# Performance work log

Measured on AMD Instinct MI355X. Metric: run time of the kernel, lower is better.

## Reference

```python
import jax, jax.numpy as jnp
import numpy as np

B, T, HOR, N = 64, 12, 12, 1024
DIN, DOUT, YCOV, H, K, E = 1, 1, 1, 64, 3, 8


def setup_inputs() -> dict:
    key = jax.random.key(0)
    ks = jax.random.split(key, 10)
    def g(k, shape, s=1.0):
        return jax.random.normal(k, shape, dtype=jnp.float32) * s
    # xavier-ish scale for GCN weights: 1/sqrt(fan_in)
    gi = 1.0 / np.sqrt(K * (DIN + H))
    di = 1.0 / np.sqrt(K * (DOUT + YCOV + H))
    return {
        "x": jax.random.uniform(ks[0], (B, T, N, DIN), dtype=jnp.float32),
        "y_cov": jax.random.uniform(ks[1], (B, HOR, N, YCOV), dtype=jnp.float32),
        "node_emb": g(ks[2], (N, E), 1.0),
        "enc_gate_W": g(ks[3], (K * (DIN + H), 2 * H), gi),
        "enc_gate_b": jnp.zeros((2 * H,), jnp.float32),
        "enc_upd_W": g(ks[4], (K * (DIN + H), H), gi),
        "enc_upd_b": jnp.zeros((H,), jnp.float32),
        "dec_gate_W": g(ks[5], (K * (DOUT + YCOV + H), 2 * H), di),
        "dec_gate_b": jnp.zeros((2 * H,), jnp.float32),
        "dec_upd_W": g(ks[6], (K * (DOUT + YCOV + H), H), di),
        "dec_upd_b": jnp.zeros((H,), jnp.float32),
        "proj_W": g(ks[7], (H, DOUT), 1.0 / np.sqrt(H)),
        "proj_b": jnp.zeros((DOUT,), jnp.float32),
    }


def _cheb_supports(A):
    # support_set = [I, A, 2*A@A - I, ...], cheb_k terms
    s = [jnp.eye(A.shape[0], dtype=A.dtype), A]
    for _ in range(2, K):
        s.append(2.0 * A @ s[-1] - s[-2])
    return jnp.stack(s)  # [K, N, N]


def _gcn(x, sup, W, b):
    # x: [B,N,C]; sup: [K,N,N]; matches torch cat([s_k @ x], -1) ordering (k-major)
    bb, nn, cc = x.shape
    xg = jnp.einsum('knm,bmc->bnkc', sup, x).reshape(bb, nn, K * cc)
    return xg @ W + b


def _cell(x, h, sup, gW, gb, uW, ub):
    zr = jax.nn.sigmoid(_gcn(jnp.concatenate([x, h], -1), sup, gW, gb))
    z, r = jnp.split(zr, 2, axis=-1)
    hc = jnp.tanh(_gcn(jnp.concatenate([x, z * h], -1), sup, uW, ub))
    return r * h + (1.0 - r) * hc


def reference(x, y_cov, node_emb, enc_gate_W, enc_gate_b, enc_upd_W, enc_upd_b,
              dec_gate_W, dec_gate_b, dec_upd_W, dec_upd_b, proj_W, proj_b):
    # adaptive adjacency from node embeddings (AGCRN-style)
    A = jax.nn.softmax(jax.nn.relu(node_emb @ node_emb.T), axis=-1)
    sup = _cheb_supports(A)

    h0 = jnp.zeros((B, N, H), x.dtype)

    def enc_step(h, xt):
        h2 = _cell(xt, h, sup, enc_gate_W, enc_gate_b, enc_upd_W, enc_upd_b)
        return h2, None
    h_enc, _ = jax.lax.scan(enc_step, h0, jnp.swapaxes(x, 0, 1))  # final state [B,N,H]

    go0 = jnp.zeros((B, N, DOUT), x.dtype)

    def dec_step(carry, yt):
        h, go = carry
        h2 = _cell(jnp.concatenate([go, yt], -1), h, sup,
                   dec_gate_W, dec_gate_b, dec_upd_W, dec_upd_b)
        go2 = h2 @ proj_W + proj_b
        return (h2, go2), go2
    _, outs = jax.lax.scan(dec_step, (h_enc, go0), jnp.swapaxes(y_cov, 0, 1))
    return jnp.swapaxes(outs, 0, 1)  # [B, HOR, N, DOUT]
```

## Files before the change

### kernel.cpp

```cpp
#include <hip/hip_runtime.h>
#include <math.h>

constexpr int N = 1024, B = 64, T = 12, HOR = 12, H = 64, E = 8;
constexpr size_t NBH = 4194304;

constexpr size_t A_off   = 0;
constexpr size_t Pxy_off = 1048576;
constexpr size_t h_off   = Pxy_off + 3145728;
constexpr size_t Ph_off  = h_off + NBH;
constexpr size_t zh_off  = Ph_off + 2 * NBH;
constexpr size_t r_off   = zh_off + NBH;
constexpr size_t go_off  = r_off + NBH;
constexpr size_t A2_off  = go_off + 65536;
constexpr size_t Bth_off = A2_off + 1048576;
constexpr size_t Btz_off = Bth_off + 2162688;
constexpr size_t xyK_off = Btz_off + 2097152;
constexpr size_t Pgo_off = xyK_off + 786432;
constexpr size_t wp_off  = Pgo_off + 131072;

typedef __attribute__((ext_vector_type(8))) short short8;
typedef _Float16 half8 __attribute__((ext_vector_type(8)));
typedef __attribute__((ext_vector_type(4))) float f32x4;

__device__ __forceinline__ unsigned f2bf(float x) {
  unsigned u = __float_as_uint(x);
  return (u + 0x7fffu + ((u >> 16) & 1u)) >> 16;
}
__device__ __forceinline__ float bf2f(unsigned h) {
  return __uint_as_float(h << 16);
}
__device__ __forceinline__ ushort f2h(float x) {
  _Float16 h = (_Float16)x;
  ushort u;
  __builtin_memcpy(&u, &h, 2);
  return u;
}
__device__ __forceinline__ void split4(float4 v, uint2& hi, uint2& lo) {
  unsigned h0 = f2bf(v.x), h1 = f2bf(v.y), h2 = f2bf(v.z), h3 = f2bf(v.w);
  unsigned l0 = f2bf(v.x - bf2f(h0)), l1 = f2bf(v.y - bf2f(h1));
  unsigned l2 = f2bf(v.z - bf2f(h2)), l3 = f2bf(v.w - bf2f(h3));
  hi.x = (h0 & 0xffffu) | (h1 << 16); hi.y = (h2 & 0xffffu) | (h3 << 16);
  lo.x = (l0 & 0xffffu) | (l1 << 16); lo.y = (l2 & 0xffffu) | (l3 << 16);
}

typedef const __attribute__((address_space(1))) void gas_t;
typedef __attribute__((address_space(3))) void las_t;

__global__ __launch_bounds__(256) void build_A(const float* __restrict__ emb,
                                               float* __restrict__ A) {
  __shared__ float sE[N * E];
  __shared__ float sv[N];
  __shared__ float rmax[4], rsum[4];
  const int i = blockIdx.x;
  for (int idx = threadIdx.x; idx < N * E / 4; idx += 256)
    ((float4*)sE)[idx] = ((const float4*)emb)[idx];
  __syncthreads();
  float ei[E];
#pragma unroll
  for (int e = 0; e < E; ++e) ei[e] = sE[i * E + e];
  float mymax = 0.f;
  for (int j = threadIdx.x; j < N; j += 256) {
    float d = 0.f;
#pragma unroll
    for (int e = 0; e < E; ++e) d = fmaf(ei[e], sE[j * E + e], d);
    d = fmaxf(d, 0.f);
    sv[j] = d;
    mymax = fmaxf(mymax, d);
  }
  for (int off = 32; off; off >>= 1) mymax = fmaxf(mymax, __shfl_down(mymax, off));
  const int wid = threadIdx.x >> 6, lid = threadIdx.x & 63;
  if (lid == 0) rmax[wid] = mymax;
  __syncthreads();
  const float m = fmaxf(fmaxf(rmax[0], rmax[1]), fmaxf(rmax[2], rmax[3]));
  float mysum = 0.f;
  for (int j = threadIdx.x; j < N; j += 256) {
    float ev = expf(sv[j] - m);
    sv[j] = ev;
    mysum += ev;
  }
  for (int off = 32; off; off >>= 1) mysum += __shfl_down(mysum, off);
  if (lid == 0) rsum[wid] = mysum;
  __syncthreads();
  const float inv = 1.f / (rsum[0] + rsum[1] + rsum[2] + rsum[3]);
  for (int j = threadIdx.x; j < N; j += 256) A[i * N + j] = sv[j] * inv;
}

__global__ __launch_bounds__(256) void pack_split_S(const float* __restrict__ A,
                                                    ushort* __restrict__ L,
                                                    ushort* __restrict__ R) {
  __shared__ float tile[32][33];
  const int bx = blockIdx.x * 32;
  const int by = blockIdx.y * 32;
  const int tx = threadIdx.x & 31;
  const int tg = threadIdx.x >> 5;
#pragma unroll
  for (int p = 0; p < 4; ++p) {
    int ty = tg * 4 + p;
    tile[ty][tx] = A[(size_t)(by + ty) * 1024 + bx + tx];
  }
  __syncthreads();
#pragma unroll
  for (int p = 0; p < 4; ++p) {
    int ty = tg * 4 + p;
    float v = tile[ty][tx];
    unsigned h = f2bf(v);
    unsigned l = f2bf(v - bf2f(h));
    size_t lb = (size_t)(by + ty) * 3072 + 3 * (bx + tx);
    L[lb + 0] = (ushort)h; L[lb + 1] = (ushort)l; L[lb + 2] = (ushort)h;
    float w = tile[tx][ty];
    unsigned hh = f2bf(w);
    unsigned ll = f2bf(w - bf2f(hh));
    size_t rbi = (size_t)(bx + ty) * 3072 + 3 * (by + tx);
    R[rbi + 0] = (ushort)hh; R[rbi + 1] = (ushort)hh; R[rbi + 2] = (ushort)ll;
  }
}

__global__ __launch_bounds__(256) void conv_bf16(const float* __restrict__ src,
                                                 ushort* __restrict__ dst) {
  int i = blockIdx.x * 256 + threadIdx.x;
  float4 v = ((const float4*)src)[i];
  ushort4 o;
  o.x = (ushort)f2bf(v.x); o.y = (ushort)f2bf(v.y);
  o.z = (ushort)f2bf(v.z); o.w = (ushort)f2bf(v.w);
  ((ushort4*)dst)[i] = o;
}

__global__ __launch_bounds__(256) void conv_xyK(const float* __restrict__ src,
                                                ushort* __restrict__ dst, int off) {
  int id = blockIdx.x * 256 + threadIdx.x;
  int tb = id >> 10, n = id & 1023;
  int tt = tb >> 6, b = tb & 63;
  dst[(size_t)(off + tb) * 1024 + n] = (ushort)f2bf(src[((size_t)b * T + tt) * 1024 + n]);
}

__global__ __launch_bounds__(256) void pack_Wbf(const float* __restrict__ W,
                                                ushort* __restrict__ out,
                                                int CIN, int NC, int xoff) {
  int idx = blockIdx.x * 256 + threadIdx.x;
  int total = 2 * NC * 32;
  if (idx >= total) return;
  int kk = idx & 31;
  int rest = idx >> 5;
  int col = rest % NC;
  int half = rest / NC;
  float v = W[(size_t)(xoff + half * 32 + kk) * NC + col];
  unsigned hi = f2bf(v);
  unsigned lo = f2bf(v - bf2f(hi));
  size_t base = (size_t)(half * 2) * NC * 32;
  out[base + (size_t)col * 32 + kk] = (ushort)hi;
  out[base + (size_t)NC * 32 + (size_t)col * 32 + kk] = (ushort)lo;
}

__global__ __launch_bounds__(256) void pack_W16(const float* __restrict__ W,
                                                ushort* __restrict__ out,
                                                int CIN, int NC, int xoff) {
  int idx = blockIdx.x * 256 + threadIdx.x;
  int total = 2 * 2 * NC * 32;
  if (idx >= total) return;
  int kk = idx & 31;
  int rest = idx >> 5;
  int col = rest % NC;
  rest /= NC;
  int half = rest & 1;
  int s1 = rest >> 1;
  int s = s1 + 1;
  float v = W[(size_t)(s * CIN + xoff + half * 32 + kk) * NC + col];
  out[(size_t)(s1 * 2 + half) * NC * 32 + (size_t)col * 32 + kk] = f2h(v);
}

__global__ __launch_bounds__(256) void gemm_s2p(
    const ushort* __restrict__ L, const ushort* __restrict__ R,
    float* __restrict__ P) {
  __shared__ ushort As[128 * 32];
  __shared__ ushort Bs[128 * 32];
  const int t = threadIdx.x;
  const int wave = t >> 6, lane = t & 63;
  const int bm = blockIdx.y * 128, bn = blockIdx.x * 128;
  const int wm = (wave & 1) * 64, wn = (wave >> 1) * 64;
  float* Pz = P + (size_t)blockIdx.z * 1048576;
  const int kbase = blockIdx.z * 768;

  const ushort* aSrc[2]; const ushort* bSrc[2];
  ushort* aDst[2]; ushort* bDst[2];
#pragma unroll
  for (int u = 0; u < 2; ++u) {
    int idx = wave * 128 + u * 64 + lane;
    int row = idx >> 2;
    int kq = (idx & 3) * 8;
    aSrc[u] = L + (size_t)(bm + row) * 3072 + kq;
    bSrc[u] = R + (size_t)(bn + row) * 3072 + kq;
    aDst[u] = &As[(wave * 128 + u * 64) * 8];
    bDst[u] = &Bs[(wave * 128 + u * 64) * 8];
  }
  const int lr = lane & 15;
  const int lk = (lane >> 4) * 8;
  f32x4 acc[4][4];
#pragma unroll
  for (int i = 0; i < 4; ++i)
#pragma unroll
    for (int j = 0; j < 4; ++j) acc[i][j] = {0.f, 0.f, 0.f, 0.f};

  for (int k0 = kbase; k0 < kbase + 768; k0 += 32) {
#pragma unroll
    for (int u = 0; u < 2; ++u) {
      __builtin_amdgcn_global_load_lds((gas_t*)(aSrc[u] + k0), (las_t*)aDst[u], 16, 0, 0);
      __builtin_amdgcn_global_load_lds((gas_t*)(bSrc[u] + k0), (las_t*)bDst[u], 16, 0, 0);
    }
    __syncthreads();
    short8 a[4], b[4];
#pragma unroll
    for (int i = 0; i < 4; ++i) a[i] = *(const short8*)&As[(wm + i * 16 + lr) * 32 + lk];
#pragma unroll
    for (int j = 0; j < 4; ++j) b[j] = *(const short8*)&Bs[(wn + j * 16 + lr) * 32 + lk];
#pragma unroll
    for (int i = 0; i < 4; ++i)
#pragma unroll
      for (int j = 0; j < 4; ++j)
        acc[i][j] = __builtin_amdgcn_mfma_f32_16x16x32_bf16(a[i], b[j], acc[i][j], 0, 0, 0);
    __syncthreads();
  }
  const int cr = (lane >> 4) * 4;
  const int cc = lane & 15;
#pragma unroll
  for (int i = 0; i < 4; ++i)
#pragma unroll
    for (int j = 0; j < 4; ++j) {
      int gm = bm + wm + i * 16 + cr;
      int gn = bn + wn + j * 16 + cc;
#pragma unroll
      for (int r = 0; r < 4; ++r)
        Pz[(size_t)(gm + r) * 1024 + gn] = acc[i][j][r];
    }
}

__global__ __launch_bounds__(256) void comb_s2(const float* __restrict__ P,
                                               ushort* __restrict__ A2) {
  int idx = blockIdx.x * 256 + threadIdx.x;
  float4 a = ((const float4*)P)[idx];
  float4 b = ((const float4*)(P + 1048576))[idx];
  float4 c = ((const float4*)(P + 2097152))[idx];
  float4 d = ((const float4*)(P + 3145728))[idx];
  int base = idx << 2;
  int m = base >> 10, c0 = base & 1023;
  float v0 = 2.f * (a.x + b.x + c.x + d.x) - (m == c0 + 0 ? 1.f : 0.f);
  float v1 = 2.f * (a.y + b.y + c.y + d.y) - (m == c0 + 1 ? 1.f : 0.f);
  float v2 = 2.f * (a.z + b.z + c.z + d.z) - (m == c0 + 2 ? 1.f : 0.f);
  float v3 = 2.f * (a.w + b.w + c.w + d.w) - (m == c0 + 3 ? 1.f : 0.f);
  ushort4 o;
  o.x = (ushort)f2bf(v0); o.y = (ushort)f2bf(v1);
  o.z = (ushort)f2bf(v2); o.w = (ushort)f2bf(v3);
  ((ushort4*)(A2 + 1048576))[idx] = o;
}

template <int CMODE>
__global__ __launch_bounds__(256) void gemm_bt(
    const ushort* __restrict__ A2, const ushort* __restrict__ Bt, int n1,
    ushort* __restrict__ C1h, float* __restrict__ C1f, float* __restrict__ C2) {
  __shared__ ushort As[2][64 * 32];
  __shared__ ushort Bs[2][128 * 32];
  const int t = threadIdx.x;
  const int wave = t >> 6, lane = t & 63;
  int bxi, byi;
  if (CMODE == 0) {
    bxi = blockIdx.x; byi = blockIdx.y;
  } else {
    int lin = blockIdx.x;
    if (lin < 1024) {
      bxi = (lin & 7) * 4 + ((lin >> 3) & 3);
      byi = lin >> 5;
    } else {
      bxi = 32; byi = lin - 1024;
    }
  }
  const int bm = byi * 64, bn = bxi * 128;
  const int wm = (wave & 1) * 32, wn = (wave >> 1) * 64;

  const ushort* aSrc; const ushort* bSrc[2];
  ushort* aDst[2]; ushort* bDst[2][2];
  {
    int idx = wave * 64 + lane;
    int row = idx >> 2;
    int kq = (idx & 3) * 8;
    aSrc = A2 + (size_t)(bm + row) * 1024 + kq;
#pragma unroll
    for (int p = 0; p < 2; ++p) aDst[p] = &As[p][(wave * 64) * 8];
  }
#pragma unroll
  for (int u = 0; u < 2; ++u) {
    int idx = wave * 128 + u * 64 + lane;
    int row = idx >> 2;
    int kq = (idx & 3) * 8;
    bSrc[u] = Bt + (size_t)(bn + row) * 1024 + kq;
#pragma unroll
    for (int p = 0; p < 2; ++p)
      bDst[p][u] = &Bs[p][(wave * 128 + u * 64) * 8];
  }
  const int lr = lane & 15, lk = (lane >> 4) * 8;
  int aOff[2], bOff[4];
#pragma unroll
  for (int i = 0; i < 2; ++i) aOff[i] = (wm + i * 16 + lr) * 32 + lk;
#pragma unroll
  for (int j = 0; j < 4; ++j) bOff[j] = (wn + j * 16 + lr) * 32 + lk;

  f32x4 acc[2][4];
#pragma unroll
  for (int i = 0; i < 2; ++i)
#pragma unroll
    for (int j = 0; j < 4; ++j) acc[i][j] = {0.f, 0.f, 0.f, 0.f};

  for (int k0 = 0; k0 < 1024; k0 += 64) {
#pragma unroll
    for (int p = 0; p < 2; ++p) {
      __builtin_amdgcn_global_load_lds((gas_t*)(aSrc + k0 + p * 32),
                                       (las_t*)aDst[p], 16, 0, 0);
#pragma unroll
      for (int u = 0; u < 2; ++u)
        __builtin_amdgcn_global_load_lds((gas_t*)(bSrc[u] + k0 + p * 32),
                                         (las_t*)bDst[p][u], 16, 0, 0);
    }
    __syncthreads();
#pragma unroll
    for (int p = 0; p < 2; ++p) {
      short8 a[2], b[4];
#pragma unroll
      for (int i = 0; i < 2; ++i) a[i] = *(const short8*)&As[p][aOff[i]];
#pragma unroll
      for (int j = 0; j < 4; ++j) b[j] = *(const short8*)&Bs[p][bOff[j]];
#pragma unroll
      for (int i = 0; i < 2; ++i)
#pragma unroll
        for (int j = 0; j < 4; ++j)
          acc[i][j] = __builtin_amdgcn_mfma_f32_16x16x32_bf16(a[i], b[j], acc[i][j], 0, 0, 0);
    }
    __syncthreads();
  }

  const int cr = (lane >> 4) * 4;
  const int cc = lane & 15;
#pragma unroll
  for (int i = 0; i < 2; ++i) {
#pragma unroll
    for (int j = 0; j < 4; ++j) {
      int gm = bm + wm + i * 16 + cr;
      int gn = bn + wn + j * 16 + cc;
      if (gn < n1) {
        if (CMODE == 0) {
          float* p = C1f + (size_t)gm * n1 + gn;
#pragma unroll
          for (int r = 0; r < 4; ++r) p[(size_t)r * n1] = acc[i][j][r];
        } else {
          int half = gm >> 10, nn = gm & 1023;
          ushort* p = C1h + (size_t)half * NBH +
                      ((size_t)(gn >> 6) * 1024 + nn) * 64 + (gn & 63);
#pragma unroll
          for (int r = 0; r < 4; ++r) p[(size_t)r * 64] = f2h(acc[i][j][r]);
        }
      } else if (C2 != nullptr && gn < n1 + 64) {
        float* p = C2 + (size_t)gm * 64 + (gn - n1);
#pragma unroll
        for (int r = 0; r < 4; ++r) p[(size_t)r * 64] = acc[i][j][r];
      }
    }
  }
}

template <int NX>
__global__ __launch_bounds__(256, 4) void gate_mfma(
    const float* __restrict__ hmat, const ushort* __restrict__ Ph16,
    const ushort* __restrict__ Wbf, const ushort* __restrict__ W16,
    const float* __restrict__ Wf, const float* __restrict__ bias,
    const float* __restrict__ xb0, int xbs0, const float* __restrict__ xp0, int xs0,
    const float* __restrict__ xb1, int xbs1, const float* __restrict__ xp1, int xs1,
    float* __restrict__ zh, float* __restrict__ rbuf, ushort* __restrict__ Btz) {
  constexpr int CIN = NX + 64;
  __shared__ ushort smem[12288];
  ushort* Ah = smem;
  ushort* Al = smem + 2048;
  ushort* Bh = smem + 4096;
  ushort* Bl = smem + 8192;
  ushort* A16 = smem;
  ushort* B16 = smem + 4096;
  ushort* transT = smem;
  __shared__ float sxv[3][2][64];
  __shared__ float sWx[3][2][128];
  const int t = threadIdx.x;
  const int wave = t >> 6, lane = t & 63;
  const int bm = blockIdx.x * 64;
  const int wm = (wave & 1) * 32, wn = (wave >> 1) * 64;
  const int lr = lane & 15, lk = (lane >> 4) * 8;

  if (t < 64) {
    int grow = bm + t;
    int n = grow & 1023, b = grow >> 10;
    sxv[0][0][t] = xb0[(size_t)b * xbs0 + n];
    sxv[1][0][t] = xp0[(size_t)n * xs0 + b];
    sxv[2][0][t] = xp0[(size_t)1024 * xs0 + (size_t)n * xs0 + b];
    if (NX == 2) {
      sxv[0][1][t] = xb1[(size_t)b * xbs1 + n];
      sxv[1][1][t] = xp1[(size_t)n * xs1 + b];
      sxv[2][1][t] = xp1[(size_t)1024 * xs1 + (size_t)n * xs1 + b];
    }
  } else if (t < 192) {
    int col = t - 64;
#pragma unroll
    for (int s = 0; s < 3; ++s)
#pragma unroll
      for (int f = 0; f < NX; ++f)
        sWx[s][f][col] = Wf[(size_t)(s * CIN + f) * 128 + col];
  }

  int arow[2], ajq[2];
#pragma unroll
  for (int p = 0; p < 2; ++p) {
    int f = p * 256 + t;
    arow[p] = f >> 3;
    ajq[p] = (f & 7) * 4;
  }
  const int hrow = t >> 2, hjq = (t & 3) * 8;

  float4 pf[2];
#pragma unroll
  for (int p = 0; p < 2; ++p)
    pf[p] = *(const float4*)(hmat + (size_t)(bm + arow[p]) * 64 + ajq[p]);
  uint4 px;

  f32x4 acc[2][4];
#pragma unroll
  for (int i = 0; i < 2; ++i)
#pragma unroll
    for (int j = 0; j < 4; ++j) acc[i][j] = {0.f, 0.f, 0.f, 0.f};

#pragma unroll
  for (int half = 0; half < 2; ++half) {
#pragma unroll
    for (int p = 0; p < 2; ++p) {
      uint2 hi, lo;
      split4(pf[p], hi, lo);
      *(uint2*)&Ah[arow[p] * 32 + ajq[p]] = hi;
      *(uint2*)&Al[arow[p] * 32 + ajq[p]] = lo;
    }
    const ushort* wph = Wbf + (size_t)(half * 2) * (128 * 32);
    const ushort* wpl = wph + 128 * 32;
#pragma unroll
    for (int u = 0; u < 2; ++u) {
      int idx = wave * 128 + u * 64 + lane;
      __builtin_amdgcn_global_load_lds((gas_t*)(wph + idx * 8), (las_t*)&Bh[idx * 8], 16, 0, 0);
      __builtin_amdgcn_global_load_lds((gas_t*)(wpl + idx * 8), (las_t*)&Bl[idx * 8], 16, 0, 0);
    }
    __syncthreads();
    if (half == 0) {
#pragma unroll
      for (int p = 0; p < 2; ++p)
        pf[p] = *(const float4*)(hmat + (size_t)(bm + arow[p]) * 64 + 32 + ajq[p]);
    } else {
      px = *(const uint4*)(Ph16 + (size_t)(bm + hrow) * 64 + hjq);
    }
    short8 ah[2], al[2], bh[4], bl[4];
#pragma unroll
    for (int i = 0; i < 2; ++i) {
      ah[i] = *(const short8*)&Ah[(wm + i * 16 + lr) * 32 + lk];
      al[i] = *(const short8*)&Al[(wm + i * 16 + lr) * 32 + lk];
    }
#pragma unroll
    for (int j = 0; j < 4; ++j) {
      bh[j] = *(const short8*)&Bh[(wn + j * 16 + lr) * 32 + lk];
      bl[j] = *(const short8*)&Bl[(wn + j * 16 + lr) * 32 + lk];
    }
#pragma unroll
    for (int i = 0; i < 2; ++i)
#pragma unroll
      for (int j = 0; j < 4; ++j) {
        acc[i][j] = __builtin_amdgcn_mfma_f32_16x16x32_bf16(ah[i], bh[j], acc[i][j], 0, 0, 0);
        acc[i][j] = __builtin_amdgcn_mfma_f32_16x16x32_bf16(al[i], bh[j], acc[i][j], 0, 0, 0);
        acc[i][j] = __builtin_amdgcn_mfma_f32_16x16x32_bf16(ah[i], bl[j], acc[i][j], 0, 0, 0);
      }
    __syncthreads();
  }

  for (int it = 0; it < 4; ++it) {
    const int s1 = it >> 1, half = it & 1;
    *(uint4*)&A16[hrow * 32 + hjq] = px;
    const ushort* w16 = W16 + (size_t)(s1 * 2 + half) * (128 * 32);
#pragma unroll
    for (int u = 0; u < 2; ++u) {
      int idx = wave * 128 + u * 64 + lane;
      __builtin_amdgcn_global_load_lds((gas_t*)(w16 + idx * 8), (las_t*)&B16[idx * 8], 16, 0, 0);
    }
    __syncthreads();
    if (it < 3) {
      const int nit = it + 1;
      const ushort* src = Ph16 + (size_t)(nit >> 1) * NBH;
      px = *(const uint4*)(src + (size_t)(bm + hrow) * 64 + (nit & 1) * 32 + hjq);
    }
    half8 a16[2], b16[4];
#pragma unroll
    for (int i = 0; i < 2; ++i)
      a16[i] = *(const half8*)&A16[(wm + i * 16 + lr) * 32 + lk];
#pragma unroll
    for (int j = 0; j < 4; ++j)
      b16[j] = *(const half8*)&B16[(wn + j * 16 + lr) * 32 + lk];
#pragma unroll
    for (int i = 0; i < 2; ++i)
#pragma unroll
      for (int j = 0; j < 4; ++j)
        acc[i][j] = __builtin_amdgcn_mfma_f32_16x16x32_f16(a16[i], b16[j], acc[i][j], 0, 0, 0);
    __syncthreads();
  }

  const int cr = (lane >> 4) * 4;
  const int cc = lane & 15;
#pragma unroll
  for (int i = 0; i < 2; ++i) {
#pragma unroll
    for (int j = 0; j < 4; ++j) {
      int col = wn + j * 16 + cc;
      float bcol = bias[col];
#pragma unroll
      for (int r = 0; r < 4; ++r) {
        int rowl = wm + i * 16 + cr + r;
        int grow = bm + rowl;
        float v = acc[i][j][r] + bcol;
#pragma unroll
        for (int s = 0; s < 3; ++s)
#pragma unroll
          for (int f = 0; f < NX; ++f)
            v = fmaf(sxv[s][f][rowl], sWx[s][f][col], v);
        float sig = 1.f / (1.f + expf(-v));
        if (col < 64) {
          float zv = sig * hmat[(size_t)grow * 64 + col];
          zh[(size_t)grow * 64 + col] = zv;
          transT[col * 72 + rowl] = (ushort)f2bf(zv);
        } else {
          rbuf[(size_t)grow * 64 + col - 64] = sig;
        }
      }
    }
  }
  __syncthreads();
  const int bq = bm >> 10, nb = bm & 1023;
  for (int idx = t; idx < 512; idx += 256) {
    int j = idx >> 3, ch = idx & 7;
    uint4 v = *(const uint4*)&transT[j * 72 + ch * 8];
    *(uint4*)(Btz + (((size_t)(bq * 64 + j)) << 10) + nb + ch * 8) = v;
  }
}

template <int NX, int PROJ>
__global__ __launch_bounds__(256, 4) void upd_mfma(
    float* __restrict__ hmat, const float* __restrict__ zhb, const ushort* __restrict__ Pzh16,
    const ushort* __restrict__ Wbf, const ushort* __restrict__ W16,
    const float* __restrict__ Wf, const float* __restrict__ bias,
    const float* __restrict__ xb0, int xbs0, const float* __restrict__ xp0, int xs0,
    const float* __restrict__ xb1, int xbs1, const float* __restrict__ xp1, int xs1,
    const float* __restrict__ rbuf, ushort* __restrict__ Bth,
    const float* __restrict__ pW, const float* __restrict__ pb,
    float* __restrict__ gobuf, float* __restrict__ outp, int tstep) {
  constexpr int CIN = NX + 64;
  __shared__ ushort smem[8192];
  ushort* Ah = smem;
  ushort* Al = smem + 2048;
  ushort* Bh = smem + 4096;
  ushort* Bl = smem + 6144;
  ushort* A16 = smem;
  ushort* B16 = smem + 4096;
  ushort* transT = smem;
  __shared__ float sxv[3][2][64];
  __shared__ float sWx[3][2][64];
  __shared__ float part[2][64];
  const int t = threadIdx.x;
  const int wave = t >> 6, lane = t & 63;
  const int bm = blockIdx.x * 64;
  const int wm = (wave & 1) * 32, wn = (wave >> 1) * 32;
  const int lr = lane & 15, lk = (lane >> 4) * 8;

  if (t < 64) {
    int grow = bm + t;
    int n = grow & 1023, b = grow >> 10;
    sxv[0][0][t] = xb0[(size_t)b * xbs0 + n];
    sxv[1][0][t] = xp0[(size_t)n * xs0 + b];
    sxv[2][0][t] = xp0[(size_t)1024 * xs0 + (size_t)n * xs0 + b];
    if (NX == 2) {
      sxv[0][1][t] = xb1[(size_t)b * xbs1 + n];
      sxv[1][1][t] = xp1[(size_t)n * xs1 + b];
      sxv[2][1][t] = xp1[(size_t)1024 * xs1 + (size_t)n * xs1 + b];
    }
  } else if (t < 128) {
    int col = t - 64;
#pragma unroll
    for (int s = 0; s < 3; ++s)
#pragma unroll
      for (int f = 0; f < NX; ++f)
        sWx[s][f][col] = Wf[(size_t)(s * CIN + f) * 64 + col];
  }

  int arow[2], ajq[2];
#pragma unroll
  for (int p = 0; p < 2; ++p) {
    int f = p * 256 + t;
    arow[p] = f >> 3;
    ajq[p] = (f & 7) * 4;
  }
  const int hrow = t >> 2, hjq = (t & 3) * 8;

  float4 pf[2];
#pragma unroll
  for (int p = 0; p < 2; ++p)
    pf[p] = *(const float4*)(zhb + (size_t)(bm + arow[p]) * 64 + ajq[p]);
  uint4 px;

  f32x4 acc[2][2];
#pragma unroll
  for (int i = 0; i < 2; ++i)
#pragma unroll
    for (int j = 0; j < 2; ++j) acc[i][j] = {0.f, 0.f, 0.f, 0.f};

#pragma unroll
  for (int half = 0; half < 2; ++half) {
#pragma unroll
    for (int p = 0; p < 2; ++p) {
      uint2 hi, lo;
      split4(pf[p], hi, lo);
      *(uint2*)&Ah[arow[p] * 32 + ajq[p]] = hi;
      *(uint2*)&Al[arow[p] * 32 + ajq[p]] = lo;
    }
    const ushort* wph = Wbf + (size_t)(half * 2) * (64 * 32);
    const ushort* wpl = wph + 64 * 32;
    {
      int idx = wave * 64 + lane;
      __builtin_amdgcn_global_load_lds((gas_t*)(wph + idx * 8), (las_t*)&Bh[idx * 8], 16, 0, 0);
      __builtin_amdgcn_global_load_lds((gas_t*)(wpl + idx * 8), (las_t*)&Bl[idx * 8], 16, 0, 0);
    }
    __syncthreads();
    if (half == 0) {
#pragma unroll
      for (int p = 0; p < 2; ++p)
        pf[p] = *(const float4*)(zhb + (size_t)(bm + arow[p]) * 64 + 32 + ajq[p]);
    } else {
      px = *(const uint4*)(Pzh16 + (size_t)(bm + hrow) * 64 + hjq);
    }
    short8 ah[2], al[2], bh[2], bl[2];
#pragma unroll
    for (int i = 0; i < 2; ++i) {
      ah[i] = *(const short8*)&Ah[(wm + i * 16 + lr) * 32 + lk];
      al[i] = *(const short8*)&Al[(wm + i * 16 + lr) * 32 + lk];
    }
#pragma unroll
    for (int j = 0; j < 2; ++j) {
      bh[j] = *(const short8*)&Bh[(wn + j * 16 + lr) * 32 + lk];
      bl[j] = *(const short8*)&Bl[(wn + j * 16 + lr) * 32 + lk];
    }
#pragma unroll
    for (int i = 0; i < 2; ++i)
#pragma unroll
      for (int j = 0; j < 2; ++j) {
        acc[i][j] = __builtin_amdgcn_mfma_f32_16x16x32_bf16(ah[i], bh[j], acc[i][j], 0, 0, 0);
        acc[i][j] = __builtin_amdgcn_mfma_f32_16x16x32_bf16(al[i], bh[j], acc[i][j], 0, 0, 0);
        acc[i][j] = __builtin_amdgcn_mfma_f32_16x16x32_bf16(ah[i], bl[j], acc[i][j], 0, 0, 0);
      }
    __syncthreads();
  }

  for (int it = 0; it < 4; ++it) {
    const int s1 = it >> 1, half = it & 1;
    *(uint4*)&A16[hrow * 32 + hjq] = px;
    const ushort* w16 = W16 + (size_t)(s1 * 2 + half) * (64 * 32);
    {
      int idx = wave * 64 + lane;
      __builtin_amdgcn_global_load_lds((gas_t*)(w16 + idx * 8), (las_t*)&B16[idx * 8], 16, 0, 0);
    }
    __syncthreads();
    if (it < 3) {
      const int nit = it + 1;
      const ushort* src = Pzh16 + (size_t)(nit >> 1) * NBH;
      px = *(const uint4*)(src + (size_t)(bm + hrow) * 64 + (nit & 1) * 32 + hjq);
    }
    half8 a16[2], b16[2];
#pragma unroll
    for (int i = 0; i < 2; ++i)
      a16[i] = *(const half8*)&A16[(wm + i * 16 + lr) * 32 + lk];
#pragma unroll
    for (int j = 0; j < 2; ++j)
      b16[j] = *(const half8*)&B16[(wn + j * 16 + lr) * 32 + lk];
#pragma unroll
    for (int i = 0; i < 2; ++i)
#pragma unroll
      for (int j = 0; j < 2; ++j)
        acc[i][j] = __builtin_amdgcn_mfma_f32_16x16x32_f16(a16[i], b16[j], acc[i][j], 0, 0, 0);
    __syncthreads();
  }

  const int cr = (lane >> 4) * 4;
  const int cc = lane & 15;
  float psv[2][4];
#pragma unroll
  for (int i = 0; i < 2; ++i)
#pragma unroll
    for (int r = 0; r < 4; ++r) psv[i][r] = 0.f;

#pragma unroll
  for (int i = 0; i < 2; ++i) {
#pragma unroll
    for (int j = 0; j < 2; ++j) {
      int col = wn + j * 16 + cc;
      float bcol = bias[col];
      float pwc = PROJ ? pW[col] : 0.f;
#pragma unroll
      for (int r = 0; r < 4; ++r) {
        int rowl = wm + i * 16 + cr + r;
        int grow = bm + rowl;
        float v = acc[i][j][r] + bcol;
#pragma unroll
        for (int s = 0; s < 3; ++s)
#pragma unroll
          for (int f = 0; f < NX; ++f)
            v = fmaf(sxv[s][f][rowl], sWx[s][f][col], v);
        float hc = tanhf(v);
        size_t idx = (size_t)grow * 64 + col;
        float rr = rbuf[idx];
        float ho = hmat[idx];
        float o = rr * ho + (1.f - rr) * hc;
        hmat[idx] = o;
        transT[col * 72 + rowl] = (ushort)f2bf(o);
        if (PROJ) psv[i][r] += o * pwc;
      }
    }
  }
  if (PROJ) {
#pragma unroll
    for (int i = 0; i < 2; ++i)
#pragma unroll
      for (int r = 0; r < 4; ++r)
#pragma unroll
        for (int off = 8; off; off >>= 1)
          psv[i][r] += __shfl_down(psv[i][r], off, 16);
    if (cc == 0) {
#pragma unroll
      for (int i = 0; i < 2; ++i)
#pragma unroll
        for (int r = 0; r < 4; ++r)
          part[wn >> 5][wm + i * 16 + cr + r] = psv[i][r];
    }
  }
  __syncthreads();
  const int bq = bm >> 10, nb = bm & 1023;
  for (int idx = t; idx < 512; idx += 256) {
    int j = idx >> 3, ch = idx & 7;
    uint4 v = *(const uint4*)&transT[j * 72 + ch * 8];
    *(uint4*)(Bth + (((size_t)(bq * 64 + j)) << 10) + nb + ch * 8) = v;
  }
  if (PROJ && t < 64) {
    int grow = bm + t;
    int n = grow & 1023, b = grow >> 10;
    float g = part[0][t] + part[1][t] + pb[0];
    gobuf[grow] = g;
    outp[((size_t)b * HOR + tstep) * N + n] = g;
    Bth[((size_t)(4096 + b)) * 1024 + n] = (ushort)f2bf(g);
  }
}

extern "C" void kernel_launch(void* const* d_in, const int* in_sizes, int n_in,
                              void* d_out, int out_size, void* d_ws, size_t ws_size,
                              hipStream_t stream) {
  const float* x    = (const float*)d_in[0];
  const float* ycov = (const float*)d_in[1];
  const float* emb  = (const float*)d_in[2];
  const float* egW  = (const float*)d_in[3];
  const float* egb  = (const float*)d_in[4];
  const float* euW  = (const float*)d_in[5];
  const float* eub  = (const float*)d_in[6];
  const float* dgW  = (const float*)d_in[7];
  const float* dgb  = (const float*)d_in[8];
  const float* duW  = (const float*)d_in[9];
  const float* dub  = (const float*)d_in[10];
  const float* pW   = (const float*)d_in[11];
  const float* pb   = (const float*)d_in[12];
  float* out = (float*)d_out;
  float* ws  = (float*)d_ws;

  float* Amat = ws + A_off;
  float* Pxy  = ws + Pxy_off;
  float* hmat = ws + h_off;
  ushort* Ph16 = (ushort*)(ws + Ph_off);
  float* zh   = ws + zh_off;
  float* rb   = ws + r_off;
  float* gob  = ws + go_off;
  float* Pgo  = ws + Pgo_off;
  ushort* A2   = (ushort*)(ws + A2_off);
  ushort* Bth  = (ushort*)(ws + Bth_off);
  ushort* Btz  = (ushort*)(ws + Btz_off);
  ushort* xyK  = (ushort*)(ws + xyK_off);
  ushort* AspL = (ushort*)(ws + zh_off);
  ushort* AspR = (ushort*)(ws + r_off);
  float*  Pp   = ws + Ph_off;
  ushort* WB   = (ushort*)(ws + wp_off);
  ushort* WbfGE = WB;
  ushort* WbfGD = WB + 16384;
  ushort* WbfUE = WB + 32768;
  ushort* WbfUD = WB + 40960;
  ushort* W16GE = WB + 49152;
  ushort* W16GD = WB + 65536;
  ushort* W16UE = WB + 81920;
  ushort* W16UD = WB + 90112;

  build_A<<<N, 256, 0, stream>>>(emb, Amat);
  pack_split_S<<<dim3(32, 32), 256, 0, stream>>>(Amat, AspL, AspR);
  gemm_s2p<<<dim3(8, 8, 4), 256, 0, stream>>>(AspL, AspR, Pp);
  comb_s2<<<1024, 256, 0, stream>>>(Pp, A2);
  conv_bf16<<<1024, 256, 0, stream>>>(Amat, A2);
  conv_xyK<<<3072, 256, 0, stream>>>(x, xyK, 0);
  conv_xyK<<<3072, 256, 0, stream>>>(ycov, xyK, 768);
  pack_Wbf<<<32, 256, 0, stream>>>(egW, WbfGE, 65, 128, 1);
  pack_Wbf<<<32, 256, 0, stream>>>(dgW, WbfGD, 66, 128, 2);
  pack_Wbf<<<16, 256, 0, stream>>>(euW, WbfUE, 65, 64, 1);
  pack_Wbf<<<16, 256, 0, stream>>>(duW, WbfUD, 66, 64, 2);
  pack_W16<<<64, 256, 0, stream>>>(egW, W16GE, 65, 128, 1);
  pack_W16<<<64, 256, 0, stream>>>(dgW, W16GD, 66, 128, 2);
  pack_W16<<<32, 256, 0, stream>>>(euW, W16UE, 65, 64, 1);
  pack_W16<<<32, 256, 0, stream>>>(duW, W16UD, 66, 64, 2);
  gemm_bt<0><<<dim3(12, 32), 256, 0, stream>>>(A2, xyK, 1536, nullptr, Pxy, nullptr);
  (void)hipMemsetAsync(hmat, 0, NBH * sizeof(float), stream);
  (void)hipMemsetAsync(Ph16, 0, 2 * NBH * sizeof(ushort), stream);
  (void)hipMemsetAsync(gob, 0, 65536 * sizeof(float), stream);
  (void)hipMemsetAsync(Bth + (size_t)4096 * 1024, 0, 128 * 1024 * sizeof(ushort), stream);

  for (int t = 0; t < T; ++t) {
    if (t > 0)
      gemm_bt<1><<<1024, 256, 0, stream>>>(A2, Bth, 4096, Ph16, nullptr, nullptr);
    gate_mfma<1><<<1024, 256, 0, stream>>>(hmat, Ph16, WbfGE, W16GE, egW, egb,
                                           x + t * 1024, T * 1024, Pxy + t * 64, 1536,
                                           nullptr, 0, nullptr, 0, zh, rb, Btz);
    if (t > 0)
      gemm_bt<1><<<1024, 256, 0, stream>>>(A2, Btz, 4096, Ph16, nullptr, nullptr);
    upd_mfma<1, 0><<<1024, 256, 0, stream>>>(hmat, zh, Ph16, WbfUE, W16UE, euW, eub,
                                             x + t * 1024, T * 1024, Pxy + t * 64, 1536,
                                             nullptr, 0, nullptr, 0, rb, Bth,
                                             nullptr, nullptr, nullptr, nullptr, 0);
  }

  for (int t = 0; t < HOR; ++t) {
    gemm_bt<1><<<1056, 256, 0, stream>>>(A2, Bth, 4096, Ph16, nullptr, Pgo);
    gate_mfma<2><<<1024, 256, 0, stream>>>(hmat, Ph16, WbfGD, W16GD, dgW, dgb,
                                           gob, 1024, Pgo, 64,
                                           ycov + t * 1024, HOR * 1024,
                                           Pxy + 768 + t * 64, 1536, zh, rb, Btz);
    gemm_bt<1><<<1024, 256, 0, stream>>>(A2, Btz, 4096, Ph16, nullptr, nullptr);
    upd_mfma<2, 1><<<1024, 256, 0, stream>>>(hmat, zh, Ph16, WbfUD, W16UD, duW, dub,
                                             gob, 1024, Pgo, 64,
                                             ycov + t * 1024, HOR * 1024,
                                             Pxy + 768 + t * 64, 1536,
                                             rb, Bth, pW, pb, gob, out, t);
  }
}
```

Baseline: 2.583 ms.

## Double-buffer LDS tiles in gemm_bt to overlap global loads with MFMA

The bf16 GEMM kernel now keeps two LDS stages for the A and B tiles. It issues the async global-to-LDS loads for the next K-chunk before computing on the current one, which also removes the trailing barrier from each iteration. The goal is to hide global memory latency behind the MFMA work. In exchange, LDS use per block doubles, which can lower occupancy.

```diff
diff --git a/kernel.cpp b/kernel.cpp
--- a/kernel.cpp
+++ b/kernel.cpp
@@ -256,8 +256,8 @@
 __global__ __launch_bounds__(256) void gemm_bt(
     const ushort* __restrict__ A2, const ushort* __restrict__ Bt, int n1,
     ushort* __restrict__ C1h, float* __restrict__ C1f, float* __restrict__ C2) {
-  __shared__ ushort As[2][64 * 32];
-  __shared__ ushort Bs[2][128 * 32];
+  __shared__ ushort As[2][2][2048];
+  __shared__ ushort Bs[2][2][4096];
   const int t = threadIdx.x;
   const int wave = t >> 6, lane = t & 63;
   int bxi, byi;
@@ -276,25 +276,27 @@
   const int wm = (wave & 1) * 32, wn = (wave >> 1) * 64;
 
   const ushort* aSrc; const ushort* bSrc[2];
-  ushort* aDst[2]; ushort* bDst[2][2];
   {
     int idx = wave * 64 + lane;
-    int row = idx >> 2;
-    int kq = (idx & 3) * 8;
-    aSrc = A2 + (size_t)(bm + row) * 1024 + kq;
-#pragma unroll
-    for (int p = 0; p < 2; ++p) aDst[p] = &As[p][(wave * 64) * 8];
+    aSrc = A2 + (size_t)(bm + (idx >> 2)) * 1024 + (idx & 3) * 8;
   }
 #pragma unroll
   for (int u = 0; u < 2; ++u) {
     int idx = wave * 128 + u * 64 + lane;
-    int row = idx >> 2;
-    int kq = (idx & 3) * 8;
-    bSrc[u] = Bt + (size_t)(bn + row) * 1024 + kq;
-#pragma unroll
-    for (int p = 0; p < 2; ++p)
-      bDst[p][u] = &Bs[p][(wave * 128 + u * 64) * 8];
-  }
+    bSrc[u] = Bt + (size_t)(bn + (idx >> 2)) * 1024 + (idx & 3) * 8;
+  }
+  ushort* aD[2][2];
+  ushort* bD[2][2][2];
+#pragma unroll
+  for (int st = 0; st < 2; ++st)
+#pragma unroll
+    for (int p = 0; p < 2; ++p) {
+      aD[st][p] = &As[st][p][wave * 64 * 8];
+#pragma unroll
+      for (int u = 0; u < 2; ++u)
+        bD[st][p][u] = &Bs[st][p][(wave * 128 + u * 64) * 8];
+    }
+
   const int lr = lane & 15, lk = (lane >> 4) * 8;
   int aOff[2], bOff[4];
 #pragma unroll
@@ -308,31 +310,36 @@
 #pragma unroll
     for (int j = 0; j < 4; ++j) acc[i][j] = {0.f, 0.f, 0.f, 0.f};
 
-  for (int k0 = 0; k0 < 1024; k0 += 64) {
+  auto issue = [&](int k0, int st) {
 #pragma unroll
     for (int p = 0; p < 2; ++p) {
       __builtin_amdgcn_global_load_lds((gas_t*)(aSrc + k0 + p * 32),
-                                       (las_t*)aDst[p], 16, 0, 0);
+                                       (las_t*)aD[st][p], 16, 0, 0);
 #pragma unroll
       for (int u = 0; u < 2; ++u)
         __builtin_amdgcn_global_load_lds((gas_t*)(bSrc[u] + k0 + p * 32),
-                                         (las_t*)bDst[p][u], 16, 0, 0);
-    }
-    __syncthreads();
+                                         (las_t*)bD[st][p][u], 16, 0, 0);
+    }
+  };
+
+  issue(0, 0);
+  for (int it = 0; it < 16; ++it) {
+    const int st = it & 1;
+    __syncthreads();
+    if (it + 1 < 16) issue((it + 1) * 64, st ^ 1);
 #pragma unroll
     for (int p = 0; p < 2; ++p) {
       short8 a[2], b[4];
 #pragma unroll
-      for (int i = 0; i < 2; ++i) a[i] = *(const short8*)&As[p][aOff[i]];
-#pragma unroll
-      for (int j = 0; j < 4; ++j) b[j] = *(const short8*)&Bs[p][bOff[j]];
+      for (int i = 0; i < 2; ++i) a[i] = *(const short8*)&As[st][p][aOff[i]];
+#pragma unroll
+      for (int j = 0; j < 4; ++j) b[j] = *(const short8*)&Bs[st][p][bOff[j]];
 #pragma unroll
       for (int i = 0; i < 2; ++i)
 #pragma unroll
         for (int j = 0; j < 4; ++j)
           acc[i][j] = __builtin_amdgcn_mfma_f32_16x16x32_bf16(a[i], b[j], acc[i][j], 0, 0, 0);
     }
-    __syncthreads();
   }
 
   const int cr = (lane >> 4) * 4;
```

Result: slower. 2.989 ms (+15.7%).

## Load GEMM fragments directly from global into registers, dropping LDS staging

Applied to the files above, without the earlier changes.

The bf16 GEMM kernel no longer stages A and B tiles through shared memory with global_load_lds and barriers. Each wave now loads its MFMA fragments straight from global memory into registers, software-pipelined with a two-stage register double buffer. This removes the LDS traffic and the __syncthreads pairs per k-step. In exchange, tile data shared across waves is fetched redundantly from global/L2, and the 16-byte per-lane strided row reads coalesce less well.

```diff
diff --git a/kernel.cpp b/kernel.cpp
--- a/kernel.cpp
+++ b/kernel.cpp
@@ -256,8 +256,6 @@
 __global__ __launch_bounds__(256) void gemm_bt(
     const ushort* __restrict__ A2, const ushort* __restrict__ Bt, int n1,
     ushort* __restrict__ C1h, float* __restrict__ C1f, float* __restrict__ C2) {
-  __shared__ ushort As[2][64 * 32];
-  __shared__ ushort Bs[2][128 * 32];
   const int t = threadIdx.x;
   const int wave = t >> 6, lane = t & 63;
   int bxi, byi;
@@ -274,33 +272,17 @@
   }
   const int bm = byi * 64, bn = bxi * 128;
   const int wm = (wave & 1) * 32, wn = (wave >> 1) * 64;
-
-  const ushort* aSrc; const ushort* bSrc[2];
-  ushort* aDst[2]; ushort* bDst[2][2];
-  {
-    int idx = wave * 64 + lane;
-    int row = idx >> 2;
-    int kq = (idx & 3) * 8;
-    aSrc = A2 + (size_t)(bm + row) * 1024 + kq;
-#pragma unroll
-    for (int p = 0; p < 2; ++p) aDst[p] = &As[p][(wave * 64) * 8];
-  }
-#pragma unroll
-  for (int u = 0; u < 2; ++u) {
-    int idx = wave * 128 + u * 64 + lane;
-    int row = idx >> 2;
-    int kq = (idx & 3) * 8;
-    bSrc[u] = Bt + (size_t)(bn + row) * 1024 + kq;
-#pragma unroll
-    for (int p = 0; p < 2; ++p)
-      bDst[p][u] = &Bs[p][(wave * 128 + u * 64) * 8];
-  }
-  const int lr = lane & 15, lk = (lane >> 4) * 8;
-  int aOff[2], bOff[4];
-#pragma unroll
-  for (int i = 0; i < 2; ++i) aOff[i] = (wm + i * 16 + lr) * 32 + lk;
-#pragma unroll
-  for (int j = 0; j < 4; ++j) bOff[j] = (wn + j * 16 + lr) * 32 + lk;
+  const int lr = lane & 15;
+  const int lk8 = (lane >> 4) * 8;
+
+  const ushort* aRow[2];
+#pragma unroll
+  for (int i = 0; i < 2; ++i)
+    aRow[i] = A2 + (size_t)(bm + wm + i * 16 + lr) * 1024 + lk8;
+  const ushort* bRow[4];
+#pragma unroll
+  for (int j = 0; j < 4; ++j)
+    bRow[j] = Bt + (size_t)(bn + wn + j * 16 + lr) * 1024 + lk8;
 
   f32x4 acc[2][4];
 #pragma unroll
@@ -308,31 +290,34 @@
 #pragma unroll
     for (int j = 0; j < 4; ++j) acc[i][j] = {0.f, 0.f, 0.f, 0.f};
 
+  short8 a0[2], b0[4], a1[2], b1[4];
+#pragma unroll
+  for (int i = 0; i < 2; ++i) a0[i] = *(const short8*)(aRow[i]);
+#pragma unroll
+  for (int j = 0; j < 4; ++j) b0[j] = *(const short8*)(bRow[j]);
+
+#pragma unroll 4
   for (int k0 = 0; k0 < 1024; k0 += 64) {
 #pragma unroll
-    for (int p = 0; p < 2; ++p) {
-      __builtin_amdgcn_global_load_lds((gas_t*)(aSrc + k0 + p * 32),
-                                       (las_t*)aDst[p], 16, 0, 0);
-#pragma unroll
-      for (int u = 0; u < 2; ++u)
-        __builtin_amdgcn_global_load_lds((gas_t*)(bSrc[u] + k0 + p * 32),
-                                         (las_t*)bDst[p][u], 16, 0, 0);
-    }
-    __syncthreads();
-#pragma unroll
-    for (int p = 0; p < 2; ++p) {
-      short8 a[2], b[4];
-#pragma unroll
-      for (int i = 0; i < 2; ++i) a[i] = *(const short8*)&As[p][aOff[i]];
-#pragma unroll
-      for (int j = 0; j < 4; ++j) b[j] = *(const short8*)&Bs[p][bOff[j]];
-#pragma unroll
-      for (int i = 0; i < 2; ++i)
-#pragma unroll
-        for (int j = 0; j < 4; ++j)
-          acc[i][j] = __builtin_amdgcn_mfma_f32_16x16x32_bf16(a[i], b[j], acc[i][j], 0, 0, 0);
-    }
-    __syncthreads();
+    for (int i = 0; i < 2; ++i) a1[i] = *(const short8*)(aRow[i] + k0 + 32);
+#pragma unroll
+    for (int j = 0; j < 4; ++j) b1[j] = *(const short8*)(bRow[j] + k0 + 32);
+#pragma unroll
+    for (int i = 0; i < 2; ++i)
+#pragma unroll
+      for (int j = 0; j < 4; ++j)
+        acc[i][j] = __builtin_amdgcn_mfma_f32_16x16x32_bf16(a0[i], b0[j], acc[i][j], 0, 0, 0);
+    if (k0 + 64 < 1024) {
+#pragma unroll
+      for (int i = 0; i < 2; ++i) a0[i] = *(const short8*)(aRow[i] + k0 + 64);
+#pragma unroll
+      for (int j = 0; j < 4; ++j) b0[j] = *(const short8*)(bRow[j] + k0 + 64);
+    }
+#pragma unroll
+    for (int i = 0; i < 2; ++i)
+#pragma unroll
+      for (int j = 0; j < 4; ++j)
+        acc[i][j] = __builtin_amdgcn_mfma_f32_16x16x32_bf16(a1[i], b1[j], acc[i][j], 0, 0, 0);
   }
 
   const int cr = (lane >> 4) * 4;
```

Measured after the change: 5.497 ms. +112.8%, slower.
